# Optimization experiments

Hardware: AMD Instinct MI355X
Metric: run time of the kernel (lower is better)

Reference implementation:

```python
import jax, jax.numpy as jnp
import numpy as np

B, N, D = 2, 2048, 1024
H, DH = 16, 64
INNER = H * DH  # 1024
EPS = 1e-5


def setup_inputs() -> dict:
    key = jax.random.key(0)
    ks = jax.random.split(key, 7)
    x = jax.random.normal(ks[0], (B, N, D), dtype=jnp.float32)
    mask = jax.random.uniform(ks[1], (B, N)) < 0.9
    mask = mask.at[:, 0].set(True)  # guarantee at least one valid key per row
    attn_bias = jax.random.normal(ks[2], (H, N, N), dtype=jnp.float32) * 0.02
    ln_w = jnp.ones((D,), dtype=jnp.float32)
    ln_b = jnp.zeros((D,), dtype=jnp.float32)
    wq = jax.random.normal(ks[3], (D, INNER), dtype=jnp.float32) * 0.02
    wkv = jax.random.normal(ks[4], (D, 2 * DH), dtype=jnp.float32) * 0.02
    wo = jax.random.normal(ks[5], (INNER, D), dtype=jnp.float32) * 0.02
    return {"x": x, "attn_bias": attn_bias, "ln_w": ln_w, "ln_b": ln_b,
            "wq": wq, "wkv": wkv, "wo": wo, "mask": mask}


def reference(x, attn_bias, ln_w, ln_b, wq, wkv, wo, mask):
    scale = DH ** -0.5
    # NOTE: in the torch module, kv_input = x BEFORE self.norm (context=None),
    # so K/V come from raw x while Q comes from LayerNorm(x).
    mu = jnp.mean(x, axis=-1, keepdims=True)
    var = jnp.var(x, axis=-1, keepdims=True)
    xn = (x - mu) / jnp.sqrt(var + EPS) * ln_w + ln_b
    q = (xn @ wq).reshape(B, N, H, DH).transpose(0, 2, 1, 3) * scale  # b h n d
    kv = x @ wkv                     # b n 2*dh (shared single KV head, MQA)
    k, v = kv[..., :DH], kv[..., DH:]
    sim = jnp.einsum('bhid,bjd->bhij', q, k) + attn_bias  # bias broadcasts over b
    mask_value = -jnp.finfo(sim.dtype).max
    sim = jnp.where(mask[:, None, None, :], sim, mask_value)
    attn = jax.nn.softmax(sim, axis=-1)
    out = jnp.einsum('bhij,bjd->bhid', attn, v)
    out = out.transpose(0, 2, 1, 3).reshape(B, N, INNER)
    return out @ wo
```

## Files before the change

### kernel.cpp

```cpp
#include <hip/hip_runtime.h>
#include <hip/hip_bf16.h>

typedef __bf16 bf16_t;
typedef __bf16 bf16x4 __attribute__((ext_vector_type(4)));
typedef __bf16 bf16x8 __attribute__((ext_vector_type(8)));
typedef float f32x4 __attribute__((ext_vector_type(4)));

static constexpr int BB    = 2;
static constexpr int SEQ   = 2048;
static constexpr int DM    = 1024;
static constexpr int NHEAD = 16;
static constexpr int HD    = 64;
static constexpr float L2E = 1.4426950408889634f;

__device__ __forceinline__ bf16x8 ld8(const bf16_t* p) {
  return *reinterpret_cast<const bf16x8*>(p);
}

__device__ __forceinline__ void gl_lds16(const bf16_t* g, bf16_t* l) {
  __builtin_amdgcn_global_load_lds(
      (const __attribute__((address_space(1))) void*)g,
      (__attribute__((address_space(3))) void*)l, 16, 0, 0);
}

__device__ __forceinline__ uint2 shfl2(uint2 v, int src) {
  uint2 r;
  r.x = (unsigned)__shfl((int)v.x, src, 64);
  r.y = (unsigned)__shfl((int)v.y, src, 64);
  return r;
}

template <typename T> __device__ __forceinline__ T cvt_out(float v);
template <> __device__ __forceinline__ float  cvt_out<float >(float v) { return v; }
template <> __device__ __forceinline__ bf16_t cvt_out<bf16_t>(float v) { return (bf16_t)v; }

__global__ __launch_bounds__(256) void transpose_cast(const float* __restrict__ in,
                                                      bf16_t* __restrict__ out,
                                                      int R, int C) {
  __shared__ float tile[32][33];
  const int c0 = blockIdx.x * 32, r0 = blockIdx.y * 32;
  const int tx = threadIdx.x & 31, ty = threadIdx.x >> 5;
#pragma unroll
  for (int y = ty; y < 32; y += 8)
    tile[y][tx] = in[(size_t)(r0 + y) * C + (c0 + tx)];
  __syncthreads();
#pragma unroll
  for (int y = ty; y < 32; y += 8)
    out[(size_t)(c0 + y) * R + (r0 + tx)] = (bf16_t)tile[tx][y];
}

__global__ __launch_bounds__(256) void row_prep(const float* __restrict__ x,
    const float* __restrict__ ln_w, const float* __restrict__ ln_b,
    const int* __restrict__ mask,
    bf16_t* __restrict__ xbf, bf16_t* __restrict__ xn, float* __restrict__ maskA) {
  const int row = blockIdx.x, t = threadIdx.x;
  __shared__ float red[8];
  const float4 xv = *reinterpret_cast<const float4*>(&x[(size_t)row * DM + t * 4]);
  float s  = xv.x + xv.y + xv.z + xv.w;
  float s2 = xv.x * xv.x + xv.y * xv.y + xv.z * xv.z + xv.w * xv.w;
#pragma unroll
  for (int off = 32; off >= 1; off >>= 1) {
    s  += __shfl_xor(s,  off, 64);
    s2 += __shfl_xor(s2, off, 64);
  }
  if ((t & 63) == 0) { red[t >> 6] = s; red[4 + (t >> 6)] = s2; }
  __syncthreads();
  s  = red[0] + red[1] + red[2] + red[3];
  s2 = red[4] + red[5] + red[6] + red[7];
  const float mu   = s * (1.0f / DM);
  const float var  = s2 * (1.0f / DM) - mu * mu;
  const float rstd = rsqrtf(var + 1e-5f);
  const float4 wv = *reinterpret_cast<const float4*>(&ln_w[t * 4]);
  const float4 bv = *reinterpret_cast<const float4*>(&ln_b[t * 4]);
  union { bf16_t h[4]; uint2 u; } p0, p1;
  p0.h[0] = (bf16_t)xv.x; p0.h[1] = (bf16_t)xv.y;
  p0.h[2] = (bf16_t)xv.z; p0.h[3] = (bf16_t)xv.w;
  p1.h[0] = (bf16_t)((xv.x - mu) * rstd * wv.x + bv.x);
  p1.h[1] = (bf16_t)((xv.y - mu) * rstd * wv.y + bv.y);
  p1.h[2] = (bf16_t)((xv.z - mu) * rstd * wv.z + bv.z);
  p1.h[3] = (bf16_t)((xv.w - mu) * rstd * wv.w + bv.w);
  *reinterpret_cast<uint2*>(&xbf[(size_t)row * DM + t * 4]) = p0.u;
  *reinterpret_cast<uint2*>(&xn [(size_t)row * DM + t * 4]) = p1.u;
  if (t == 0) maskA[row] = mask[row] ? 0.0f : -1e30f;
}

__device__ __forceinline__ void gemm_core_db(
    const bf16_t* __restrict__ A, const bf16_t* __restrict__ Bt, int K,
    int m0, int n0, bf16_t* As, bf16_t* Bs, f32x4 (&acc)[4][4]) {
  const int t = threadIdx.x, lane = t & 63, w = t >> 6;
  const int wm = (w & 1) * 64, wn = (w >> 1) * 64;
  const int l15 = lane & 15, q4 = lane >> 4;
  const int sr = lane >> 2, sc = (lane & 3) * 8;
  const bf16_t* Ap0 = A  + (size_t)(m0 + w * 32 + sr) * K + sc;
  const bf16_t* Ap1 = Ap0 + (size_t)16 * K;
  const bf16_t* Bp0 = Bt + (size_t)(n0 + w * 32 + sr) * K + sc;
  const bf16_t* Bp1 = Bp0 + (size_t)16 * K;
  const int la0 = (w * 32) * 32, la1 = (w * 32 + 16) * 32;
  gl_lds16(Ap0, As + la0);
  gl_lds16(Ap1, As + la1);
  gl_lds16(Bp0, Bs + la0);
  gl_lds16(Bp1, Bs + la1);
  __syncthreads();
  int buf = 0;
  for (int k0 = 0; k0 < K; k0 += 32) {
    const int nbuf = buf ^ 1;
    if (k0 + 32 < K) {
      const int kn = k0 + 32;
      gl_lds16(Ap0 + kn, As + nbuf * (128 * 32) + la0);
      gl_lds16(Ap1 + kn, As + nbuf * (128 * 32) + la1);
      gl_lds16(Bp0 + kn, Bs + nbuf * (128 * 32) + la0);
      gl_lds16(Bp1 + kn, Bs + nbuf * (128 * 32) + la1);
    }
    const bf16_t* Asb = As + buf * (128 * 32);
    const bf16_t* Bsb = Bs + buf * (128 * 32);
    bf16x8 af[4], bfr[4];
#pragma unroll
    for (int mt = 0; mt < 4; ++mt) af[mt]  = ld8(&Asb[(wm + mt * 16 + l15) * 32 + q4 * 8]);
#pragma unroll
    for (int nt = 0; nt < 4; ++nt) bfr[nt] = ld8(&Bsb[(wn + nt * 16 + l15) * 32 + q4 * 8]);
#pragma unroll
    for (int mt = 0; mt < 4; ++mt)
#pragma unroll
      for (int nt = 0; nt < 4; ++nt)
        acc[mt][nt] = __builtin_amdgcn_mfma_f32_16x16x32_bf16(af[mt], bfr[nt], acc[mt][nt], 0, 0, 0);
    __syncthreads();
    buf = nbuf;
  }
}

__global__ __launch_bounds__(256) void gemm_qkv(
    const bf16_t* __restrict__ xn,  const bf16_t* __restrict__ wqT,  bf16_t* __restrict__ qb,
    const bf16_t* __restrict__ xbf, const bf16_t* __restrict__ wkvT,
    bf16_t* __restrict__ kkb, bf16_t* __restrict__ vTb) {
  __shared__ alignas(16) bf16_t As[2][128 * 32];
  __shared__ alignas(16) bf16_t Bs[2][128 * 32];
  const int bx = blockIdx.x;
  const bool isKV = (bx < 32);
  const int m0 = isKV ? bx * 128 : ((bx - 32) & 31) * 128;
  const int n0 = isKV ? 0 : ((bx - 32) >> 5) * 128;
  const bf16_t* A  = isKV ? xbf  : xn;
  const bf16_t* Bt = isKV ? wkvT : wqT;
  f32x4 acc[4][4] = {};
  gemm_core_db(A, Bt, DM, m0, n0, &As[0][0], &Bs[0][0], acc);

  const int lane = threadIdx.x & 63, w = threadIdx.x >> 6;
  const int wm = (w & 1) * 64, wn = (w >> 1) * 64;
  const int l15 = lane & 15, q4 = lane >> 4;
#pragma unroll
  for (int mt = 0; mt < 4; ++mt)
#pragma unroll
    for (int nt = 0; nt < 4; ++nt)
#pragma unroll
      for (int r = 0; r < 4; ++r) {
        const int gm = m0 + wm + mt * 16 + q4 * 4 + r;
        const int gn = n0 + wn + nt * 16 + l15;
        if (isKV) {
          const bf16_t ov = (bf16_t)acc[mt][nt][r];
          if (gn < HD) kkb[(size_t)gm * HD + gn] = ov;
          else vTb[((size_t)(gm >> 11) * HD + (gn - HD)) * SEQ + (gm & 2047)] = ov;
        } else {
          qb[(size_t)gm * DM + gn] = (bf16_t)(acc[mt][nt][r] * 0.125f);
        }
      }
}

__global__ __launch_bounds__(256) void gemm_out(const bf16_t* __restrict__ A,
    const bf16_t* __restrict__ Bt, float* __restrict__ C, int K) {
  __shared__ alignas(16) bf16_t As[2][128 * 32];
  __shared__ alignas(16) bf16_t Bs[2][128 * 32];
  const int m0 = blockIdx.x * 128, n0 = blockIdx.y * 128;
  f32x4 acc[4][4] = {};
  gemm_core_db(A, Bt, K, m0, n0, &As[0][0], &Bs[0][0], acc);
  const int lane = threadIdx.x & 63, w = threadIdx.x >> 6;
  const int wm = (w & 1) * 64, wn = (w >> 1) * 64;
  const int l15 = lane & 15, q4 = lane >> 4;
#pragma unroll
  for (int mt = 0; mt < 4; ++mt)
#pragma unroll
    for (int nt = 0; nt < 4; ++nt)
#pragma unroll
      for (int r = 0; r < 4; ++r) {
        const int gm = m0 + wm + mt * 16 + q4 * 4 + r;
        const int gn = n0 + wn + nt * 16 + l15;
        C[(size_t)gm * DM + gn] = acc[mt][nt][r];
      }
}

__global__ __launch_bounds__(256, 4) void flash_attn(
    const bf16_t* __restrict__ q,
    const bf16_t* __restrict__ kk,
    const bf16_t* __restrict__ vT,
    const float*  __restrict__ bias,
    const float*  __restrict__ maskA,
    bf16_t* __restrict__ aout)
{
  const int b = blockIdx.y & 1, h = blockIdx.y >> 1;
  const int i0 = blockIdx.x * 64;
  const int t = threadIdx.x, lane = t & 63, w = t >> 6;
  const int l15 = lane & 15, q4 = lane >> 4;

  __shared__ alignas(16) bf16_t Ks[2][64][72];
  __shared__ alignas(16) bf16_t Vs[2][64][72];

  const bf16_t* qrow = &q[((size_t)b * SEQ + i0 + w * 16 + l15) * DM + h * HD];
  const bf16x8 bq0 = ld8(qrow + q4 * 8);
  const bf16x8 bq1 = ld8(qrow + 32 + q4 * 8);

  f32x4 o[4] = {};
  float m_run = -1e30f, l_run = 0.0f;

  const float* bias_p = bias + (size_t)h * SEQ * SEQ
                      + (size_t)(i0 + w * 16 + l15) * SEQ + q4 * 4;
  const float* mask_p = maskA + b * SEQ + q4 * 4;

  const int sr = t >> 2, sc = (t & 3) * 16;
  const bf16_t* kp = &kk[((size_t)b * SEQ + sr) * HD + sc];
  const bf16_t* vp = &vT[((size_t)b * HD + sr) * SEQ + sc];

  uint4 kr0 = *reinterpret_cast<const uint4*>(kp);
  uint4 kr1 = *reinterpret_cast<const uint4*>(kp + 8);
  uint4 vr0 = *reinterpret_cast<const uint4*>(vp);
  uint4 vr1 = *reinterpret_cast<const uint4*>(vp + 8);
  f32x4 bm[4];
#pragma unroll
  for (int mt = 0; mt < 4; ++mt) {
    const f32x4 bv = *reinterpret_cast<const f32x4*>(bias_p + mt * 16);
    const f32x4 mv = *reinterpret_cast<const f32x4*>(mask_p + mt * 16);
    bm[mt] = bv + mv;
  }
  *reinterpret_cast<uint4*>(&Ks[0][sr][sc])     = kr0;
  *reinterpret_cast<uint4*>(&Ks[0][sr][sc + 8]) = kr1;
  *reinterpret_cast<uint4*>(&Vs[0][sr][sc])     = vr0;
  *reinterpret_cast<uint4*>(&Vs[0][sr][sc + 8]) = vr1;
  __syncthreads();

  for (int it = 0; it < SEQ / 64; ++it) {
    const int buf = it & 1;
    const int j1 = (it + 1) * 64;
    const bool more = (j1 < SEQ);
    if (more) {
      kr0 = *reinterpret_cast<const uint4*>(kp + (size_t)j1 * HD);
      kr1 = *reinterpret_cast<const uint4*>(kp + (size_t)j1 * HD + 8);
      vr0 = *reinterpret_cast<const uint4*>(vp + j1);
      vr1 = *reinterpret_cast<const uint4*>(vp + j1 + 8);
    }

    f32x4 s[4];
    __builtin_amdgcn_s_setprio(1);
#pragma unroll
    for (int mt = 0; mt < 4; ++mt) {
      const bf16x8 a0 = ld8(&Ks[buf][mt * 16 + l15][q4 * 8]);
      const bf16x8 a1 = ld8(&Ks[buf][mt * 16 + l15][32 + q4 * 8]);
      f32x4 z = {0.f, 0.f, 0.f, 0.f};
      z = __builtin_amdgcn_mfma_f32_16x16x32_bf16(a0, bq0, z, 0, 0, 0);
      z = __builtin_amdgcn_mfma_f32_16x16x32_bf16(a1, bq1, z, 0, 0, 0);
      s[mt] = z;
    }
    __builtin_amdgcn_s_setprio(0);

    float mx = -1e30f;
#pragma unroll
    for (int mt = 0; mt < 4; ++mt)
#pragma unroll
      for (int r = 0; r < 4; ++r) {
        s[mt][r] = s[mt][r] + bm[mt][r];
        mx = fmaxf(mx, s[mt][r]);
      }
    if (more) {
#pragma unroll
      for (int mt = 0; mt < 4; ++mt) {
        const f32x4 bv = *reinterpret_cast<const f32x4*>(bias_p + j1 + mt * 16);
        const f32x4 mv = *reinterpret_cast<const f32x4*>(mask_p + j1 + mt * 16);
        bm[mt] = bv + mv;
      }
    }
    mx = fmaxf(mx, __shfl_xor(mx, 16, 64));
    mx = fmaxf(mx, __shfl_xor(mx, 32, 64));
    const float mnew  = fmaxf(m_run, mx);
    const float alpha = __builtin_amdgcn_exp2f((m_run - mnew) * L2E);
    const float cc    = -mnew * L2E;
    m_run = mnew;

    float su = 0.0f;
#pragma unroll
    for (int mt = 0; mt < 4; ++mt)
#pragma unroll
      for (int r = 0; r < 4; ++r) {
        s[mt][r] = __builtin_amdgcn_exp2f(__builtin_fmaf(s[mt][r], L2E, cc));
        su += s[mt][r];
      }
    su += __shfl_xor(su, 16, 64);
    su += __shfl_xor(su, 32, 64);
    l_run = l_run * alpha + su;

#pragma unroll
    for (int r = 0; r < 4; ++r) {
      const float a_r = __shfl(alpha, q4 * 4 + r, 64);
      o[0][r] *= a_r; o[1][r] *= a_r; o[2][r] *= a_r; o[3][r] *= a_r;
    }

    uint2 pk[4];
#pragma unroll
    for (int mt = 0; mt < 4; ++mt) {
      union { bf16_t hh[4]; uint2 u; } pu;
      pu.hh[0] = (bf16_t)s[mt][0]; pu.hh[1] = (bf16_t)s[mt][1];
      pu.hh[2] = (bf16_t)s[mt][2]; pu.hh[3] = (bf16_t)s[mt][3];
      pk[mt] = pu.u;
    }
    const int src0 = ((q4 & 1) << 5) + l15;
    const int src1 = src0 + 16;
    const bool hiSel = (q4 >> 1) != 0;
#pragma unroll
    for (int ks = 0; ks < 2; ++ks) {
      const uint2 a0 = shfl2(pk[2 * ks],     src0);
      const uint2 a1 = shfl2(pk[2 * ks + 1], src0);
      const uint2 b0 = shfl2(pk[2 * ks],     src1);
      const uint2 b1 = shfl2(pk[2 * ks + 1], src1);
      union { unsigned u[4]; bf16x8 v; } pf;
      pf.u[0] = hiSel ? a1.x : a0.x; pf.u[1] = hiSel ? a1.y : a0.y;
      pf.u[2] = hiSel ? b1.x : b0.x; pf.u[3] = hiSel ? b1.y : b0.y;
      __builtin_amdgcn_s_setprio(1);
#pragma unroll
      for (int nt = 0; nt < 4; ++nt) {
        const bf16x8 vv = ld8(&Vs[buf][nt * 16 + l15][ks * 32 + q4 * 8]);
        o[nt] = __builtin_amdgcn_mfma_f32_16x16x32_bf16(pf.v, vv, o[nt], 0, 0, 0);
      }
      __builtin_amdgcn_s_setprio(0);
    }

    if (more) {
      *reinterpret_cast<uint4*>(&Ks[buf ^ 1][sr][sc])     = kr0;
      *reinterpret_cast<uint4*>(&Ks[buf ^ 1][sr][sc + 8]) = kr1;
      *reinterpret_cast<uint4*>(&Vs[buf ^ 1][sr][sc])     = vr0;
      *reinterpret_cast<uint4*>(&Vs[buf ^ 1][sr][sc + 8]) = vr1;
    }
    __syncthreads();
  }

#pragma unroll
  for (int r = 0; r < 4; ++r) {
    const float linv = 1.0f / __shfl(l_run, q4 * 4 + r, 64);
    const int gi = i0 + w * 16 + q4 * 4 + r;
    bf16_t* dst = &aout[((size_t)b * SEQ + gi) * DM + h * HD];
#pragma unroll
    for (int nt = 0; nt < 4; ++nt)
      dst[nt * 16 + l15] = (bf16_t)(o[nt][r] * linv);
  }
}

extern "C" void kernel_launch(void* const* d_in, const int* in_sizes, int n_in,
                              void* d_out, int out_size, void* d_ws, size_t ws_size,
                              hipStream_t stream) {
  const float* x         = (const float*)d_in[0];
  const float* attn_bias = (const float*)d_in[1];
  const float* ln_w      = (const float*)d_in[2];
  const float* ln_b      = (const float*)d_in[3];
  const float* wq        = (const float*)d_in[4];
  const float* wkv       = (const float*)d_in[5];
  const float* wo        = (const float*)d_in[6];
  const int*   mask      = (const int*)d_in[7];
  float* out = (float*)d_out;

  char* ws = (char*)d_ws;
  size_t off = 0;
  auto alloc = [&](size_t bytes) {
    char* p = ws + off;
    off += (bytes + 255) & ~(size_t)255;
    return p;
  };
  bf16_t* xbf   = (bf16_t*)alloc((size_t)BB * SEQ * DM * 2);
  bf16_t* xn    = (bf16_t*)alloc((size_t)BB * SEQ * DM * 2);
  bf16_t* wqT   = (bf16_t*)alloc((size_t)DM * DM * 2);
  bf16_t* wkvT  = (bf16_t*)alloc((size_t)2 * HD * DM * 2);
  bf16_t* woT   = (bf16_t*)alloc((size_t)DM * DM * 2);
  bf16_t* qb    = (bf16_t*)alloc((size_t)BB * SEQ * DM * 2);
  bf16_t* kkb   = (bf16_t*)alloc((size_t)BB * SEQ * HD * 2);
  bf16_t* vTb   = (bf16_t*)alloc((size_t)BB * HD * SEQ * 2);
  bf16_t* aoutb = (bf16_t*)alloc((size_t)BB * SEQ * DM * 2);
  float*  maskA = (float*)alloc((size_t)BB * SEQ * 4);

  transpose_cast<<<dim3(DM / 32, DM / 32), 256, 0, stream>>>(wq, wqT, DM, DM);
  transpose_cast<<<dim3(128 / 32, DM / 32), 256, 0, stream>>>(wkv, wkvT, DM, 128);
  transpose_cast<<<dim3(DM / 32, DM / 32), 256, 0, stream>>>(wo, woT, DM, DM);
  row_prep<<<BB * SEQ, 256, 0, stream>>>(x, ln_w, ln_b, mask, xbf, xn, maskA);
  gemm_qkv<<<288, 256, 0, stream>>>(xn, wqT, qb, xbf, wkvT, kkb, vTb);
  flash_attn<<<dim3(SEQ / 64, BB * NHEAD), 256, 0, stream>>>(qb, kkb, vTb, attn_bias,
                                                             maskA, aoutb);
  gemm_out<<<dim3(32, 8), 256, 0, stream>>>(aoutb, woT, out, DM);
}
```

Before: 527.6 us.

## Load K/V fragments directly from global into registers, dropping LDS staging and barriers

The flash attention kernel no longer stages K and V tiles through shared memory with double buffering and __syncthreads. Each wave now loads its MFMA operand fragments for K and V straight from global memory (L2-resident, shared across the 16 heads), prefetching the next K tile into registers. Bias and mask for the next tile are loaded unconditionally, with the index wrapping to 0 on the last iteration. Launch bounds drop from 4 to 3 waves per SIMD to leave room for the extra registers, and the GEMM k-loop is marked not to unroll. The trade is removing LDS traffic and block-wide barriers at the cost of redundant global/L2 reads (every wave fetches the full K/V tiles), higher register pressure and lower occupancy.

```diff
diff --git a/kernel.cpp b/kernel.cpp
--- a/kernel.cpp
+++ b/kernel.cpp
@@ -102,6 +102,7 @@
   gl_lds16(Bp1, Bs + la1);
   __syncthreads();
   int buf = 0;
+#pragma unroll 1
   for (int k0 = 0; k0 < K; k0 += 32) {
     const int nbuf = buf ^ 1;
     if (k0 + 32 < K) {
@@ -186,7 +187,7 @@
       }
 }
 
-__global__ __launch_bounds__(256, 4) void flash_attn(
+__global__ __launch_bounds__(256, 3) void flash_attn(
     const bf16_t* __restrict__ q,
     const bf16_t* __restrict__ kk,
     const bf16_t* __restrict__ vT,
@@ -199,9 +200,6 @@
   const int t = threadIdx.x, lane = t & 63, w = t >> 6;
   const int l15 = lane & 15, q4 = lane >> 4;
 
-  __shared__ alignas(16) bf16_t Ks[2][64][72];
-  __shared__ alignas(16) bf16_t Vs[2][64][72];
-
   const bf16_t* qrow = &q[((size_t)b * SEQ + i0 + w * 16 + l15) * DM + h * HD];
   const bf16x8 bq0 = ld8(qrow + q4 * 8);
   const bf16x8 bq1 = ld8(qrow + 32 + q4 * 8);
@@ -213,14 +211,15 @@
                       + (size_t)(i0 + w * 16 + l15) * SEQ + q4 * 4;
   const float* mask_p = maskA + b * SEQ + q4 * 4;
 
-  const int sr = t >> 2, sc = (t & 3) * 16;
-  const bf16_t* kp = &kk[((size_t)b * SEQ + sr) * HD + sc];
-  const bf16_t* vp = &vT[((size_t)b * HD + sr) * SEQ + sc];
-
-  uint4 kr0 = *reinterpret_cast<const uint4*>(kp);
-  uint4 kr1 = *reinterpret_cast<const uint4*>(kp + 8);
-  uint4 vr0 = *reinterpret_cast<const uint4*>(vp);
-  uint4 vr1 = *reinterpret_cast<const uint4*>(vp + 8);
+  const bf16_t* kbase = &kk[((size_t)b * SEQ + l15) * HD + q4 * 8];
+  const bf16_t* vbase = &vT[((size_t)b * HD + l15) * SEQ + q4 * 8];
+
+  bf16x8 ka[4], kb[4];
+#pragma unroll
+  for (int mt = 0; mt < 4; ++mt) {
+    ka[mt] = ld8(kbase + (size_t)(mt * 16) * HD);
+    kb[mt] = ld8(kbase + (size_t)(mt * 16) * HD + 32);
+  }
   f32x4 bm[4];
 #pragma unroll
   for (int mt = 0; mt < 4; ++mt) {
@@ -228,35 +227,33 @@
     const f32x4 mv = *reinterpret_cast<const f32x4*>(mask_p + mt * 16);
     bm[mt] = bv + mv;
   }
-  *reinterpret_cast<uint4*>(&Ks[0][sr][sc])     = kr0;
-  *reinterpret_cast<uint4*>(&Ks[0][sr][sc + 8]) = kr1;
-  *reinterpret_cast<uint4*>(&Vs[0][sr][sc])     = vr0;
-  *reinterpret_cast<uint4*>(&Vs[0][sr][sc + 8]) = vr1;
-  __syncthreads();
-
+
+#pragma unroll 2
   for (int it = 0; it < SEQ / 64; ++it) {
-    const int buf = it & 1;
-    const int j1 = (it + 1) * 64;
-    const bool more = (j1 < SEQ);
-    if (more) {
-      kr0 = *reinterpret_cast<const uint4*>(kp + (size_t)j1 * HD);
-      kr1 = *reinterpret_cast<const uint4*>(kp + (size_t)j1 * HD + 8);
-      vr0 = *reinterpret_cast<const uint4*>(vp + j1);
-      vr1 = *reinterpret_cast<const uint4*>(vp + j1 + 8);
+    const int j0 = it * 64;
+    const int jn = (it + 1 < SEQ / 64) ? j0 + 64 : 0;
+
+    bf16x8 vv0[4], vv1[4];
+#pragma unroll
+    for (int nt = 0; nt < 4; ++nt) {
+      vv0[nt] = ld8(vbase + (size_t)(nt * 16) * SEQ + j0);
+      vv1[nt] = ld8(vbase + (size_t)(nt * 16) * SEQ + j0 + 32);
     }
 
     f32x4 s[4];
-    __builtin_amdgcn_s_setprio(1);
 #pragma unroll
     for (int mt = 0; mt < 4; ++mt) {
-      const bf16x8 a0 = ld8(&Ks[buf][mt * 16 + l15][q4 * 8]);
-      const bf16x8 a1 = ld8(&Ks[buf][mt * 16 + l15][32 + q4 * 8]);
       f32x4 z = {0.f, 0.f, 0.f, 0.f};
-      z = __builtin_amdgcn_mfma_f32_16x16x32_bf16(a0, bq0, z, 0, 0, 0);
-      z = __builtin_amdgcn_mfma_f32_16x16x32_bf16(a1, bq1, z, 0, 0, 0);
+      z = __builtin_amdgcn_mfma_f32_16x16x32_bf16(ka[mt], bq0, z, 0, 0, 0);
+      z = __builtin_amdgcn_mfma_f32_16x16x32_bf16(kb[mt], bq1, z, 0, 0, 0);
       s[mt] = z;
     }
-    __builtin_amdgcn_s_setprio(0);
+
+#pragma unroll
+    for (int mt = 0; mt < 4; ++mt) {
+      ka[mt] = ld8(kbase + (size_t)(jn + mt * 16) * HD);
+      kb[mt] = ld8(kbase + (size_t)(jn + mt * 16) * HD + 32);
+    }
 
     float mx = -1e30f;
 #pragma unroll
@@ -266,13 +263,11 @@
         s[mt][r] = s[mt][r] + bm[mt][r];
         mx = fmaxf(mx, s[mt][r]);
       }
-    if (more) {
-#pragma unroll
-      for (int mt = 0; mt < 4; ++mt) {
-        const f32x4 bv = *reinterpret_cast<const f32x4*>(bias_p + j1 + mt * 16);
-        const f32x4 mv = *reinterpret_cast<const f32x4*>(mask_p + j1 + mt * 16);
-        bm[mt] = bv + mv;
-      }
+#pragma unroll
+    for (int mt = 0; mt < 4; ++mt) {
+      const f32x4 bv = *reinterpret_cast<const f32x4*>(bias_p + jn + mt * 16);
+      const f32x4 mv = *reinterpret_cast<const f32x4*>(mask_p + jn + mt * 16);
+      bm[mt] = bv + mv;
     }
     mx = fmaxf(mx, __shfl_xor(mx, 16, 64));
     mx = fmaxf(mx, __shfl_xor(mx, 32, 64));
@@ -319,22 +314,12 @@
       union { unsigned u[4]; bf16x8 v; } pf;
       pf.u[0] = hiSel ? a1.x : a0.x; pf.u[1] = hiSel ? a1.y : a0.y;
       pf.u[2] = hiSel ? b1.x : b0.x; pf.u[3] = hiSel ? b1.y : b0.y;
-      __builtin_amdgcn_s_setprio(1);
 #pragma unroll
       for (int nt = 0; nt < 4; ++nt) {
-        const bf16x8 vv = ld8(&Vs[buf][nt * 16 + l15][ks * 32 + q4 * 8]);
+        const bf16x8 vv = (ks == 0) ? vv0[nt] : vv1[nt];
         o[nt] = __builtin_amdgcn_mfma_f32_16x16x32_bf16(pf.v, vv, o[nt], 0, 0, 0);
       }
-      __builtin_amdgcn_s_setprio(0);
-    }
-
-    if (more) {
-      *reinterpret_cast<uint4*>(&Ks[buf ^ 1][sr][sc])     = kr0;
-      *reinterpret_cast<uint4*>(&Ks[buf ^ 1][sr][sc + 8]) = kr1;
-      *reinterpret_cast<uint4*>(&Vs[buf ^ 1][sr][sc])     = vr0;
-      *reinterpret_cast<uint4*>(&Vs[buf ^ 1][sr][sc + 8]) = vr1;
-    }
-    __syncthreads();
+    }
   }
 
 #pragma unroll
```

Measured after the change: 695.3 us. 1.32x slower.
